# Kernel optimization log

Hardware: AMD Instinct MI355X
Metric: run time of the kernel (lower is better)

Reference implementation:

```python
import jax, jax.numpy as jnp
import numpy as np

NUM_NODES = 50000
FEAT_DIM = 64
HIDDEN = 128
OUT_DIM = 128
NUM_EDGES = 640000


def setup_inputs() -> dict:
    key = jax.random.key(0)
    ks = jax.random.split(key, 8)
    edge_index = jax.random.randint(ks[0], (2, NUM_EDGES), 0, NUM_NODES, dtype=jnp.int32)
    emb = jax.random.normal(ks[1], (NUM_NODES, FEAT_DIM), dtype=jnp.float32) * 0.1
    # SAGEConv: lin_l (aggregated neighbors, with bias) and lin_r (root, no bias)
    s1 = 1.0 / np.sqrt(FEAT_DIM)
    W1l = jax.random.uniform(ks[2], (HIDDEN, FEAT_DIM), jnp.float32, -s1, s1)
    b1l = jnp.zeros((HIDDEN,), jnp.float32)
    W1r = jax.random.uniform(ks[3], (HIDDEN, FEAT_DIM), jnp.float32, -s1, s1)
    s2 = 1.0 / np.sqrt(HIDDEN)
    W2l = jax.random.uniform(ks[4], (OUT_DIM, HIDDEN), jnp.float32, -s2, s2)
    b2l = jnp.zeros((OUT_DIM,), jnp.float32)
    W2r = jax.random.uniform(ks[5], (OUT_DIM, HIDDEN), jnp.float32, -s2, s2)
    return {"edge_index": edge_index, "emb": emb, "W1l": W1l, "b1l": b1l,
            "W1r": W1r, "W2l": W2l, "b2l": b2l, "W2r": W2r}


def _sage_conv(x, src, dst, Wl, bl, Wr):
    # mean-aggregate source features at target nodes, then two linear paths
    msg = x[src]                                   # [E, d]
    agg = jax.ops.segment_sum(msg, dst, num_segments=NUM_NODES)
    deg = jax.ops.segment_sum(jnp.ones((src.shape[0],), x.dtype), dst,
                              num_segments=NUM_NODES)
    mean = agg / jnp.maximum(deg, 1.0)[:, None]    # [N, d]
    return mean @ Wl.T + bl + x @ Wr.T             # [N, out]


def reference(edge_index, emb, W1l, b1l, W1r, W2l, b2l, W2r):
    src, dst = edge_index[0], edge_index[1]
    h = jax.nn.relu(_sage_conv(emb, src, dst, W1l, b1l, W1r))
    return _sage_conv(h, src, dst, W2l, b2l, W2r)
```

## Files before the change

### kernel.cpp

```cpp
#include <hip/hip_runtime.h>

#define N_NODES 50000
#define FEAT    64
#define HID     128
#define N_EDGES 640000
#define SBLK    196
#define CAP     80

typedef __attribute__((ext_vector_type(8))) short bf16x8;
typedef __attribute__((ext_vector_type(4))) float f32x4;

static __device__ __forceinline__ unsigned short f2bf(float f) {
    unsigned u = __float_as_uint(f);
    u = u + 0x7fffu + ((u >> 16) & 1u);
    return (unsigned short)(u >> 16);
}
static __device__ __forceinline__ float bflo(unsigned u) {
    return __uint_as_float(u << 16);
}
static __device__ __forceinline__ float bfhi(unsigned u) {
    return __uint_as_float(u & 0xffff0000u);
}

#define ACC8(A, v) { \
    A[0] += bflo((v).x); A[1] += bfhi((v).x); \
    A[2] += bflo((v).y); A[3] += bfhi((v).y); \
    A[4] += bflo((v).z); A[5] += bfhi((v).z); \
    A[6] += bflo((v).w); A[7] += bfhi((v).w); }

static __device__ __forceinline__ void gridbar(int* bar, int gen) {
    __syncthreads();
    if (threadIdx.x == 0) {
        __threadfence();
        int arrived = atomicAdd(&bar[0], 1);
        if (arrived == SBLK - 1) {
            atomicExch(&bar[0], 0);
            __threadfence();
            atomicExch(&bar[1], gen);
        } else {
            while (atomicAdd(&bar[1], 0) < gen) __builtin_amdgcn_s_sleep(2);
        }
        __threadfence();
    }
    __syncthreads();
}

__global__ __launch_bounds__(256) void histfill_kernel(
        const int* __restrict__ src, const int* __restrict__ dst,
        const float* __restrict__ emb,
        const float* __restrict__ W1l, const float* __restrict__ W1r,
        const float* __restrict__ W2l, const float* __restrict__ W2r,
        int* __restrict__ count, int* __restrict__ esrc,
        unsigned* __restrict__ emb_bf_u, unsigned* __restrict__ Wbf_u,
        unsigned* __restrict__ hbf_u) {
    int gtid = blockIdx.x * 256 + threadIdx.x;
    if (gtid < N_EDGES) {
        int d = dst[gtid];
        int slot = atomicAdd(&count[d], 1);
        if (slot < CAP) esrc[d * CAP + slot] = src[gtid];
    }
    for (int i = gtid; i < N_NODES * FEAT / 2; i += N_EDGES) {
        float2 v = ((const float2*)emb)[i];
        emb_bf_u[i] = ((unsigned)f2bf(v.y) << 16) | (unsigned)f2bf(v.x);
    }
    if (gtid < FEAT / 2) emb_bf_u[N_NODES * FEAT / 2 + gtid] = 0u;
    if (gtid < HID / 2)  hbf_u[N_NODES * HID / 2 + gtid]   = 0u;
    if (gtid < 24576) {
        int w = gtid * 2;
        float lo, hi;
        if (w < 8192)       { lo = W1l[w];         hi = W1l[w + 1]; }
        else if (w < 16384) { lo = W1r[w - 8192];  hi = W1r[w - 8191]; }
        else if (w < 32768) { lo = W2l[w - 16384]; hi = W2l[w - 16383]; }
        else                { lo = W2r[w - 32768]; hi = W2r[w - 32767]; }
        Wbf_u[gtid] = ((unsigned)f2bf(hi) << 16) | (unsigned)f2bf(lo);
    }
}

__global__ __launch_bounds__(256) void permk_kernel(
        const int* __restrict__ count, int* dhist, int* dcur, int* perm,
        int* bar) {
    __shared__ int lh[64];
    __shared__ int lb2[64];
    __shared__ int dstart_sh[64];
    __shared__ int scan_tmp[64];
    int t = threadIdx.x;
    int gtid = blockIdx.x * 256 + t;

    int v = (gtid < N_NODES) ? count[gtid] : 0;
    int d = v < 63 ? v : 63;
    if (t < 64) lh[t] = 0;
    __syncthreads();
    int slot = 0;
    if (gtid < N_NODES) slot = atomicAdd(&lh[d], 1);
    __syncthreads();
    if (t < 64 && lh[t] > 0) atomicAdd(&dhist[t], lh[t]);
    gridbar(bar, 1);

    int dv = (t < 64) ? dhist[t] : 0;
    if (t < 64) scan_tmp[t] = dv;
    __syncthreads();
    for (int off = 1; off < 64; off <<= 1) {
        int add = (t >= off && t < 64) ? scan_tmp[t - off] : 0;
        __syncthreads();
        if (t < 64) scan_tmp[t] += add;
        __syncthreads();
    }
    if (t < 64) dstart_sh[t] = scan_tmp[t] - dv;
    __syncthreads();
    if (t < 64 && lh[t] > 0) lb2[t] = atomicAdd(&dcur[t], lh[t]);
    __syncthreads();
    if (gtid < N_NODES)
        perm[(N_NODES - 1) - (dstart_sh[d] + lb2[d] + slot)] = gtid;
}

__global__ __launch_bounds__(256, 4) void fgemm1_kernel(
        const unsigned short* __restrict__ embb, const int* __restrict__ cnt,
        const int* __restrict__ esrc, const int* __restrict__ perm,
        const short* __restrict__ Wl, const short* __restrict__ Wr,
        const float* __restrict__ bias, unsigned short* __restrict__ hout) {
    __shared__ unsigned short smean[16][72];
    __shared__ int sidx[16][CAP];
    __shared__ int nid[16];
    int t = threadIdx.x;
    if (t < 16) nid[t] = perm[blockIdx.x * 16 + t];
    __syncthreads();

    int sub = t >> 4, fl = t & 15;
    int half = (t >> 3) & 1, fo = t & 7;
    int n = nid[sub];
    int deg = cnt[n];
    int degc = deg < CAP ? deg : CAP;
    int beg = n * CAP;
    int rr = (degc + 15) & ~15;
    for (int j = fl; j < rr; j += 16)
        sidx[sub][j] = (j < degc) ? esrc[beg + j] : N_NODES;
    float acc[8] = {0,0,0,0,0,0,0,0};
    const uint4* eb4 = (const uint4*)embb;
    for (int i = 0; i < rr; i += 16) {
        uint4 v0 = eb4[(size_t)sidx[sub][i +  0 + half] * 8 + fo];
        uint4 v1 = eb4[(size_t)sidx[sub][i +  2 + half] * 8 + fo];
        uint4 v2 = eb4[(size_t)sidx[sub][i +  4 + half] * 8 + fo];
        uint4 v3 = eb4[(size_t)sidx[sub][i +  6 + half] * 8 + fo];
        uint4 v4 = eb4[(size_t)sidx[sub][i +  8 + half] * 8 + fo];
        uint4 v5 = eb4[(size_t)sidx[sub][i + 10 + half] * 8 + fo];
        uint4 v6 = eb4[(size_t)sidx[sub][i + 12 + half] * 8 + fo];
        uint4 v7 = eb4[(size_t)sidx[sub][i + 14 + half] * 8 + fo];
        ACC8(acc, v0) ACC8(acc, v1) ACC8(acc, v2) ACC8(acc, v3)
        ACC8(acc, v4) ACC8(acc, v5) ACC8(acc, v6) ACC8(acc, v7)
    }
    float dinv = 1.0f / fmaxf((float)deg, 1.0f);
    unsigned ow[4];
    #pragma unroll
    for (int k = 0; k < 4; ++k) {
        float lo = acc[2 * k];     lo += __shfl_xor(lo, 8);
        float hi = acc[2 * k + 1]; hi += __shfl_xor(hi, 8);
        ow[k] = ((unsigned)f2bf(hi * dinv) << 16) | (unsigned)f2bf(lo * dinv);
    }
    if (half == 0) {
        uint4 o4 = {ow[0], ow[1], ow[2], ow[3]};
        *(uint4*)&smean[sub][fo * 8] = o4;
    }
    __syncthreads();

    int wave = t >> 6, lane = t & 63;
    int col = lane & 15, quad = lane >> 4;
    int ncol = nid[col];
    int nt0 = wave * 2, nt1 = nt0 + 1;
    f32x4 acc0 = (f32x4){0.f,0.f,0.f,0.f}, acc1 = (f32x4){0.f,0.f,0.f,0.f};
    #pragma unroll
    for (int kb = 0; kb < FEAT; kb += 32) {
        bf16x8 am = *(const bf16x8*)&smean[col][kb + quad * 8];
        bf16x8 ax = *(const bf16x8*)(embb + (size_t)ncol * FEAT + kb + quad * 8);
        bf16x8 bl0 = *(const bf16x8*)(Wl + (nt0 * 16 + col) * FEAT + kb + quad * 8);
        bf16x8 br0 = *(const bf16x8*)(Wr + (nt0 * 16 + col) * FEAT + kb + quad * 8);
        bf16x8 bl1 = *(const bf16x8*)(Wl + (nt1 * 16 + col) * FEAT + kb + quad * 8);
        bf16x8 br1 = *(const bf16x8*)(Wr + (nt1 * 16 + col) * FEAT + kb + quad * 8);
        acc0 = __builtin_amdgcn_mfma_f32_16x16x32_bf16(am, bl0, acc0, 0, 0, 0);
        acc0 = __builtin_amdgcn_mfma_f32_16x16x32_bf16(ax, br0, acc0, 0, 0, 0);
        acc1 = __builtin_amdgcn_mfma_f32_16x16x32_bf16(am, bl1, acc1, 0, 0, 0);
        acc1 = __builtin_amdgcn_mfma_f32_16x16x32_bf16(ax, br1, acc1, 0, 0, 0);
    }
    float bv0 = bias[nt0 * 16 + col];
    float bv1 = bias[nt1 * 16 + col];
    #pragma unroll
    for (int r = 0; r < 4; ++r) {
        int node = nid[quad * 4 + r];
        hout[(size_t)node * HID + nt0 * 16 + col] = f2bf(fmaxf(acc0[r] + bv0, 0.f));
        hout[(size_t)node * HID + nt1 * 16 + col] = f2bf(fmaxf(acc1[r] + bv1, 0.f));
    }
}

__global__ __launch_bounds__(256, 4) void fgemm2_kernel(
        const unsigned short* __restrict__ hbf, const int* __restrict__ cnt,
        const int* __restrict__ esrc, const int* __restrict__ perm,
        const short* __restrict__ Wl, const short* __restrict__ Wr,
        const float* __restrict__ bias, float* __restrict__ out) {
    __shared__ unsigned short smean[16][136];
    __shared__ int sidx[16][CAP];
    __shared__ int nid[16];
    int t = threadIdx.x;
    if (t < 16) nid[t] = perm[blockIdx.x * 16 + t];
    __syncthreads();

    int sub = t >> 4, fl = t & 15;
    int n = nid[sub];
    int deg = cnt[n];
    int degc = deg < CAP ? deg : CAP;
    int beg = n * CAP;
    int rr = (degc + 7) & ~7;
    for (int j = fl; j < rr; j += 16)
        sidx[sub][j] = (j < degc) ? esrc[beg + j] : N_NODES;
    float acc[8] = {0,0,0,0,0,0,0,0};
    const uint4* hb4 = (const uint4*)hbf;
    for (int i = 0; i < rr; i += 8) {
        uint4 v0 = hb4[(size_t)sidx[sub][i + 0] * 16 + fl];
        uint4 v1 = hb4[(size_t)sidx[sub][i + 1] * 16 + fl];
        uint4 v2 = hb4[(size_t)sidx[sub][i + 2] * 16 + fl];
        uint4 v3 = hb4[(size_t)sidx[sub][i + 3] * 16 + fl];
        uint4 v4 = hb4[(size_t)sidx[sub][i + 4] * 16 + fl];
        uint4 v5 = hb4[(size_t)sidx[sub][i + 5] * 16 + fl];
        uint4 v6 = hb4[(size_t)sidx[sub][i + 6] * 16 + fl];
        uint4 v7 = hb4[(size_t)sidx[sub][i + 7] * 16 + fl];
        ACC8(acc, v0) ACC8(acc, v1) ACC8(acc, v2) ACC8(acc, v3)
        ACC8(acc, v4) ACC8(acc, v5) ACC8(acc, v6) ACC8(acc, v7)
    }
    float dinv = 1.0f / fmaxf((float)deg, 1.0f);
    unsigned ow[4];
    #pragma unroll
    for (int k = 0; k < 4; ++k) {
        float lo = acc[2 * k] * dinv;
        float hi = acc[2 * k + 1] * dinv;
        ow[k] = ((unsigned)f2bf(hi) << 16) | (unsigned)f2bf(lo);
    }
    uint4 o4 = {ow[0], ow[1], ow[2], ow[3]};
    *(uint4*)&smean[sub][fl * 8] = o4;
    __syncthreads();

    int wave = t >> 6, lane = t & 63;
    int col = lane & 15, quad = lane >> 4;
    int ncol = nid[col];
    int nt0 = wave * 2, nt1 = nt0 + 1;
    f32x4 acc0 = (f32x4){0.f,0.f,0.f,0.f}, acc1 = (f32x4){0.f,0.f,0.f,0.f};
    #pragma unroll
    for (int kb = 0; kb < HID; kb += 32) {
        bf16x8 am = *(const bf16x8*)&smean[col][kb + quad * 8];
        bf16x8 ax = *(const bf16x8*)(hbf + (size_t)ncol * HID + kb + quad * 8);
        bf16x8 bl0 = *(const bf16x8*)(Wl + (nt0 * 16 + col) * HID + kb + quad * 8);
        bf16x8 br0 = *(const bf16x8*)(Wr + (nt0 * 16 + col) * HID + kb + quad * 8);
        bf16x8 bl1 = *(const bf16x8*)(Wl + (nt1 * 16 + col) * HID + kb + quad * 8);
        bf16x8 br1 = *(const bf16x8*)(Wr + (nt1 * 16 + col) * HID + kb + quad * 8);
        acc0 = __builtin_amdgcn_mfma_f32_16x16x32_bf16(am, bl0, acc0, 0, 0, 0);
        acc0 = __builtin_amdgcn_mfma_f32_16x16x32_bf16(ax, br0, acc0, 0, 0, 0);
        acc1 = __builtin_amdgcn_mfma_f32_16x16x32_bf16(am, bl1, acc1, 0, 0, 0);
        acc1 = __builtin_amdgcn_mfma_f32_16x16x32_bf16(ax, br1, acc1, 0, 0, 0);
    }
    float bv0 = bias[nt0 * 16 + col];
    float bv1 = bias[nt1 * 16 + col];
    #pragma unroll
    for (int r = 0; r < 4; ++r) {
        int node = nid[quad * 4 + r];
        out[(size_t)node * HID + nt0 * 16 + col] = acc0[r] + bv0;
        out[(size_t)node * HID + nt1 * 16 + col] = acc1[r] + bv1;
    }
}

extern "C" void kernel_launch(void* const* d_in, const int* in_sizes, int n_in,
                              void* d_out, int out_size, void* d_ws, size_t ws_size,
                              hipStream_t stream) {
    const int*   edge_index = (const int*)d_in[0];
    const float* emb        = (const float*)d_in[1];
    const float* W1l        = (const float*)d_in[2];
    const float* b1l        = (const float*)d_in[3];
    const float* W1r        = (const float*)d_in[4];
    const float* W2l        = (const float*)d_in[5];
    const float* b2l        = (const float*)d_in[6];
    const float* W2r        = (const float*)d_in[7];
    float* out = (float*)d_out;

    const int* src = edge_index;
    const int* dst = edge_index + N_EDGES;

    int* iws    = (int*)d_ws;
    int* count  = iws;
    int* dhist  = iws + 50000;
    int* dcur   = iws + 50064;
    int* bar    = iws + 50128;
    int* perm   = iws + 50132;
    int* esrc   = iws + 100132;
    unsigned short* W1l_bf = (unsigned short*)(iws + 4100132);
    unsigned short* W1r_bf = (unsigned short*)(iws + 4104228);
    unsigned short* W2l_bf = (unsigned short*)(iws + 4108324);
    unsigned short* W2r_bf = (unsigned short*)(iws + 4116516);
    unsigned short* Wbf    = W1l_bf;
    unsigned short* emb_bf = (unsigned short*)(iws + 4124708);
    unsigned short* hbf    = (unsigned short*)(iws + 5724740);

    (void)hipMemsetAsync(count, 0, (size_t)50132 * sizeof(int), stream);

    histfill_kernel<<<(N_EDGES + 255) / 256, 256, 0, stream>>>(
        src, dst, emb, W1l, W1r, W2l, W2r, count, esrc,
        (unsigned*)emb_bf, (unsigned*)Wbf, (unsigned*)hbf);
    permk_kernel<<<SBLK, 256, 0, stream>>>(
        count, dhist, dcur, perm, bar);

    fgemm1_kernel<<<N_NODES / 16, 256, 0, stream>>>(
        emb_bf, count, esrc, perm,
        (const short*)W1l_bf, (const short*)W1r_bf, b1l, hbf);
    fgemm2_kernel<<<N_NODES / 16, 256, 0, stream>>>(
        hbf, count, esrc, perm,
        (const short*)W2l_bf, (const short*)W2r_bf, b2l, out);
}
```

Before: 219.1 us.

## Fuse all stages into one persistent kernel with grid barriers

Replaces the histogram/fill, permutation, and two gather+GEMM kernels with a single persistent kernel of 256 blocks of 1024 threads, separated by software grid barriers. Each block processes four 16-node tiles at once over several rounds. This removes kernel launch gaps and inter-kernel drain, but adds barrier latency and reduces the number of resident waves available to hide gather latency.

```diff
diff --git a/kernel.cpp b/kernel.cpp
--- a/kernel.cpp
+++ b/kernel.cpp
@@ -4,7 +4,10 @@
 #define FEAT    64
 #define HID     128
 #define N_EDGES 640000
-#define SBLK    196
+#define MBLK    256
+#define MTHR    1024
+#define NT      3125
+#define NROUND  4
 #define CAP     80
 
 typedef __attribute__((ext_vector_type(8))) short bf16x8;
@@ -33,7 +36,7 @@
     if (threadIdx.x == 0) {
         __threadfence();
         int arrived = atomicAdd(&bar[0], 1);
-        if (arrived == SBLK - 1) {
+        if (arrived == MBLK - 1) {
             atomicExch(&bar[0], 0);
             __threadfence();
             atomicExch(&bar[1], gen);
@@ -45,21 +48,33 @@
     __syncthreads();
 }
 
-__global__ __launch_bounds__(256) void histfill_kernel(
+__global__ __launch_bounds__(MTHR, 4) void mega_kernel(
         const int* __restrict__ src, const int* __restrict__ dst,
         const float* __restrict__ emb,
         const float* __restrict__ W1l, const float* __restrict__ W1r,
         const float* __restrict__ W2l, const float* __restrict__ W2r,
-        int* __restrict__ count, int* __restrict__ esrc,
+        const float* __restrict__ b1l, const float* __restrict__ b2l,
+        int* __restrict__ count, int* dhist, int* dcur, int* perm,
+        int* __restrict__ esrc, int* bar,
         unsigned* __restrict__ emb_bf_u, unsigned* __restrict__ Wbf_u,
-        unsigned* __restrict__ hbf_u) {
-    int gtid = blockIdx.x * 256 + threadIdx.x;
-    if (gtid < N_EDGES) {
-        int d = dst[gtid];
+        unsigned* __restrict__ hbf_u,
+        const short* __restrict__ W1l_bf, const short* __restrict__ W1r_bf,
+        const short* __restrict__ W2l_bf, const short* __restrict__ W2r_bf,
+        float* __restrict__ out) {
+    __shared__ unsigned short smean[4][16][136];
+    __shared__ int sidx[4][16][CAP];
+    __shared__ int nid[4][16];
+    __shared__ int lh[64], lb2[64], dstart_sh[64], scan_tmp[64];
+    int t = threadIdx.x;
+    int gtid = blockIdx.x * MTHR + t;
+    const int GRID = MBLK * MTHR;
+
+    for (int e = gtid; e < N_EDGES; e += GRID) {
+        int d = dst[e];
         int slot = atomicAdd(&count[d], 1);
-        if (slot < CAP) esrc[d * CAP + slot] = src[gtid];
-    }
-    for (int i = gtid; i < N_NODES * FEAT / 2; i += N_EDGES) {
+        if (slot < CAP) esrc[d * CAP + slot] = src[e];
+    }
+    for (int i = gtid; i < N_NODES * FEAT / 2; i += GRID) {
         float2 v = ((const float2*)emb)[i];
         emb_bf_u[i] = ((unsigned)f2bf(v.y) << 16) | (unsigned)f2bf(v.x);
     }
@@ -74,193 +89,185 @@
         else                { lo = W2r[w - 32768]; hi = W2r[w - 32767]; }
         Wbf_u[gtid] = ((unsigned)f2bf(hi) << 16) | (unsigned)f2bf(lo);
     }
-}
-
-__global__ __launch_bounds__(256) void permk_kernel(
-        const int* __restrict__ count, int* dhist, int* dcur, int* perm,
-        int* bar) {
-    __shared__ int lh[64];
-    __shared__ int lb2[64];
-    __shared__ int dstart_sh[64];
-    __shared__ int scan_tmp[64];
-    int t = threadIdx.x;
-    int gtid = blockIdx.x * 256 + t;
-
-    int v = (gtid < N_NODES) ? count[gtid] : 0;
-    int d = v < 63 ? v : 63;
-    if (t < 64) lh[t] = 0;
-    __syncthreads();
-    int slot = 0;
-    if (gtid < N_NODES) slot = atomicAdd(&lh[d], 1);
-    __syncthreads();
-    if (t < 64 && lh[t] > 0) atomicAdd(&dhist[t], lh[t]);
     gridbar(bar, 1);
 
-    int dv = (t < 64) ? dhist[t] : 0;
-    if (t < 64) scan_tmp[t] = dv;
-    __syncthreads();
-    for (int off = 1; off < 64; off <<= 1) {
-        int add = (t >= off && t < 64) ? scan_tmp[t - off] : 0;
-        __syncthreads();
-        if (t < 64) scan_tmp[t] += add;
-        __syncthreads();
-    }
-    if (t < 64) dstart_sh[t] = scan_tmp[t] - dv;
-    __syncthreads();
-    if (t < 64 && lh[t] > 0) lb2[t] = atomicAdd(&dcur[t], lh[t]);
-    __syncthreads();
-    if (gtid < N_NODES)
-        perm[(N_NODES - 1) - (dstart_sh[d] + lb2[d] + slot)] = gtid;
-}
-
-__global__ __launch_bounds__(256, 4) void fgemm1_kernel(
-        const unsigned short* __restrict__ embb, const int* __restrict__ cnt,
-        const int* __restrict__ esrc, const int* __restrict__ perm,
-        const short* __restrict__ Wl, const short* __restrict__ Wr,
-        const float* __restrict__ bias, unsigned short* __restrict__ hout) {
-    __shared__ unsigned short smean[16][72];
-    __shared__ int sidx[16][CAP];
-    __shared__ int nid[16];
-    int t = threadIdx.x;
-    if (t < 16) nid[t] = perm[blockIdx.x * 16 + t];
-    __syncthreads();
-
-    int sub = t >> 4, fl = t & 15;
-    int half = (t >> 3) & 1, fo = t & 7;
-    int n = nid[sub];
-    int deg = cnt[n];
-    int degc = deg < CAP ? deg : CAP;
-    int beg = n * CAP;
-    int rr = (degc + 15) & ~15;
-    for (int j = fl; j < rr; j += 16)
-        sidx[sub][j] = (j < degc) ? esrc[beg + j] : N_NODES;
-    float acc[8] = {0,0,0,0,0,0,0,0};
-    const uint4* eb4 = (const uint4*)embb;
-    for (int i = 0; i < rr; i += 16) {
-        uint4 v0 = eb4[(size_t)sidx[sub][i +  0 + half] * 8 + fo];
-        uint4 v1 = eb4[(size_t)sidx[sub][i +  2 + half] * 8 + fo];
-        uint4 v2 = eb4[(size_t)sidx[sub][i +  4 + half] * 8 + fo];
-        uint4 v3 = eb4[(size_t)sidx[sub][i +  6 + half] * 8 + fo];
-        uint4 v4 = eb4[(size_t)sidx[sub][i +  8 + half] * 8 + fo];
-        uint4 v5 = eb4[(size_t)sidx[sub][i + 10 + half] * 8 + fo];
-        uint4 v6 = eb4[(size_t)sidx[sub][i + 12 + half] * 8 + fo];
-        uint4 v7 = eb4[(size_t)sidx[sub][i + 14 + half] * 8 + fo];
-        ACC8(acc, v0) ACC8(acc, v1) ACC8(acc, v2) ACC8(acc, v3)
-        ACC8(acc, v4) ACC8(acc, v5) ACC8(acc, v6) ACC8(acc, v7)
-    }
-    float dinv = 1.0f / fmaxf((float)deg, 1.0f);
-    unsigned ow[4];
-    #pragma unroll
-    for (int k = 0; k < 4; ++k) {
-        float lo = acc[2 * k];     lo += __shfl_xor(lo, 8);
-        float hi = acc[2 * k + 1]; hi += __shfl_xor(hi, 8);
-        ow[k] = ((unsigned)f2bf(hi * dinv) << 16) | (unsigned)f2bf(lo * dinv);
-    }
-    if (half == 0) {
-        uint4 o4 = {ow[0], ow[1], ow[2], ow[3]};
-        *(uint4*)&smean[sub][fo * 8] = o4;
-    }
-    __syncthreads();
-
-    int wave = t >> 6, lane = t & 63;
-    int col = lane & 15, quad = lane >> 4;
-    int ncol = nid[col];
-    int nt0 = wave * 2, nt1 = nt0 + 1;
-    f32x4 acc0 = (f32x4){0.f,0.f,0.f,0.f}, acc1 = (f32x4){0.f,0.f,0.f,0.f};
-    #pragma unroll
-    for (int kb = 0; kb < FEAT; kb += 32) {
-        bf16x8 am = *(const bf16x8*)&smean[col][kb + quad * 8];
-        bf16x8 ax = *(const bf16x8*)(embb + (size_t)ncol * FEAT + kb + quad * 8);
-        bf16x8 bl0 = *(const bf16x8*)(Wl + (nt0 * 16 + col) * FEAT + kb + quad * 8);
-        bf16x8 br0 = *(const bf16x8*)(Wr + (nt0 * 16 + col) * FEAT + kb + quad * 8);
-        bf16x8 bl1 = *(const bf16x8*)(Wl + (nt1 * 16 + col) * FEAT + kb + quad * 8);
-        bf16x8 br1 = *(const bf16x8*)(Wr + (nt1 * 16 + col) * FEAT + kb + quad * 8);
-        acc0 = __builtin_amdgcn_mfma_f32_16x16x32_bf16(am, bl0, acc0, 0, 0, 0);
-        acc0 = __builtin_amdgcn_mfma_f32_16x16x32_bf16(ax, br0, acc0, 0, 0, 0);
-        acc1 = __builtin_amdgcn_mfma_f32_16x16x32_bf16(am, bl1, acc1, 0, 0, 0);
-        acc1 = __builtin_amdgcn_mfma_f32_16x16x32_bf16(ax, br1, acc1, 0, 0, 0);
-    }
-    float bv0 = bias[nt0 * 16 + col];
-    float bv1 = bias[nt1 * 16 + col];
-    #pragma unroll
-    for (int r = 0; r < 4; ++r) {
-        int node = nid[quad * 4 + r];
-        hout[(size_t)node * HID + nt0 * 16 + col] = f2bf(fmaxf(acc0[r] + bv0, 0.f));
-        hout[(size_t)node * HID + nt1 * 16 + col] = f2bf(fmaxf(acc1[r] + bv1, 0.f));
-    }
-}
-
-__global__ __launch_bounds__(256, 4) void fgemm2_kernel(
-        const unsigned short* __restrict__ hbf, const int* __restrict__ cnt,
-        const int* __restrict__ esrc, const int* __restrict__ perm,
-        const short* __restrict__ Wl, const short* __restrict__ Wr,
-        const float* __restrict__ bias, float* __restrict__ out) {
-    __shared__ unsigned short smean[16][136];
-    __shared__ int sidx[16][CAP];
-    __shared__ int nid[16];
-    int t = threadIdx.x;
-    if (t < 16) nid[t] = perm[blockIdx.x * 16 + t];
-    __syncthreads();
-
-    int sub = t >> 4, fl = t & 15;
-    int n = nid[sub];
-    int deg = cnt[n];
-    int degc = deg < CAP ? deg : CAP;
-    int beg = n * CAP;
-    int rr = (degc + 7) & ~7;
-    for (int j = fl; j < rr; j += 16)
-        sidx[sub][j] = (j < degc) ? esrc[beg + j] : N_NODES;
-    float acc[8] = {0,0,0,0,0,0,0,0};
-    const uint4* hb4 = (const uint4*)hbf;
-    for (int i = 0; i < rr; i += 8) {
-        uint4 v0 = hb4[(size_t)sidx[sub][i + 0] * 16 + fl];
-        uint4 v1 = hb4[(size_t)sidx[sub][i + 1] * 16 + fl];
-        uint4 v2 = hb4[(size_t)sidx[sub][i + 2] * 16 + fl];
-        uint4 v3 = hb4[(size_t)sidx[sub][i + 3] * 16 + fl];
-        uint4 v4 = hb4[(size_t)sidx[sub][i + 4] * 16 + fl];
-        uint4 v5 = hb4[(size_t)sidx[sub][i + 5] * 16 + fl];
-        uint4 v6 = hb4[(size_t)sidx[sub][i + 6] * 16 + fl];
-        uint4 v7 = hb4[(size_t)sidx[sub][i + 7] * 16 + fl];
-        ACC8(acc, v0) ACC8(acc, v1) ACC8(acc, v2) ACC8(acc, v3)
-        ACC8(acc, v4) ACC8(acc, v5) ACC8(acc, v6) ACC8(acc, v7)
-    }
-    float dinv = 1.0f / fmaxf((float)deg, 1.0f);
-    unsigned ow[4];
-    #pragma unroll
-    for (int k = 0; k < 4; ++k) {
-        float lo = acc[2 * k] * dinv;
-        float hi = acc[2 * k + 1] * dinv;
-        ow[k] = ((unsigned)f2bf(hi) << 16) | (unsigned)f2bf(lo);
-    }
-    uint4 o4 = {ow[0], ow[1], ow[2], ow[3]};
-    *(uint4*)&smean[sub][fl * 8] = o4;
-    __syncthreads();
-
-    int wave = t >> 6, lane = t & 63;
-    int col = lane & 15, quad = lane >> 4;
-    int ncol = nid[col];
-    int nt0 = wave * 2, nt1 = nt0 + 1;
-    f32x4 acc0 = (f32x4){0.f,0.f,0.f,0.f}, acc1 = (f32x4){0.f,0.f,0.f,0.f};
-    #pragma unroll
-    for (int kb = 0; kb < HID; kb += 32) {
-        bf16x8 am = *(const bf16x8*)&smean[col][kb + quad * 8];
-        bf16x8 ax = *(const bf16x8*)(hbf + (size_t)ncol * HID + kb + quad * 8);
-        bf16x8 bl0 = *(const bf16x8*)(Wl + (nt0 * 16 + col) * HID + kb + quad * 8);
-        bf16x8 br0 = *(const bf16x8*)(Wr + (nt0 * 16 + col) * HID + kb + quad * 8);
-        bf16x8 bl1 = *(const bf16x8*)(Wl + (nt1 * 16 + col) * HID + kb + quad * 8);
-        bf16x8 br1 = *(const bf16x8*)(Wr + (nt1 * 16 + col) * HID + kb + quad * 8);
-        acc0 = __builtin_amdgcn_mfma_f32_16x16x32_bf16(am, bl0, acc0, 0, 0, 0);
-        acc0 = __builtin_amdgcn_mfma_f32_16x16x32_bf16(ax, br0, acc0, 0, 0, 0);
-        acc1 = __builtin_amdgcn_mfma_f32_16x16x32_bf16(am, bl1, acc1, 0, 0, 0);
-        acc1 = __builtin_amdgcn_mfma_f32_16x16x32_bf16(ax, br1, acc1, 0, 0, 0);
-    }
-    float bv0 = bias[nt0 * 16 + col];
-    float bv1 = bias[nt1 * 16 + col];
-    #pragma unroll
-    for (int r = 0; r < 4; ++r) {
-        int node = nid[quad * 4 + r];
-        out[(size_t)node * HID + nt0 * 16 + col] = acc0[r] + bv0;
-        out[(size_t)node * HID + nt1 * 16 + col] = acc1[r] + bv1;
+    {
+        int v = (gtid < N_NODES) ? count[gtid] : 0;
+        int d = v < 63 ? v : 63;
+        if (t < 64) lh[t] = 0;
+        __syncthreads();
+        int slot = 0;
+        if (gtid < N_NODES) slot = atomicAdd(&lh[d], 1);
+        __syncthreads();
+        if (t < 64 && lh[t] > 0) atomicAdd(&dhist[t], lh[t]);
+        gridbar(bar, 2);
+        int dv = (t < 64) ? dhist[t] : 0;
+        if (t < 64) scan_tmp[t] = dv;
+        __syncthreads();
+        for (int off = 1; off < 64; off <<= 1) {
+            int add = (t >= off && t < 64) ? scan_tmp[t - off] : 0;
+            __syncthreads();
+            if (t < 64) scan_tmp[t] += add;
+            __syncthreads();
+        }
+        if (t < 64) dstart_sh[t] = scan_tmp[t] - dv;
+        __syncthreads();
+        if (t < 64 && lh[t] > 0) lb2[t] = atomicAdd(&dcur[t], lh[t]);
+        __syncthreads();
+        if (gtid < N_NODES)
+            perm[(N_NODES - 1) - (dstart_sh[d] + lb2[d] + slot)] = gtid;
+    }
+    gridbar(bar, 3);
+
+    int q = t >> 8, tq = t & 255;
+
+    {
+        int sub = tq >> 4, fl = tq & 15;
+        int half = (tq >> 3) & 1, fo = tq & 7;
+        const unsigned short* embb = (const unsigned short*)emb_bf_u;
+        const uint4* eb4 = (const uint4*)embb;
+        for (int r = 0; r < NROUND; ++r) {
+            int tile = r * (MBLK * 4) + blockIdx.x * 4 + q;
+            bool active = tile < NT;
+            if (active && tq < 16) nid[q][tq] = perm[tile * 16 + tq];
+            __syncthreads();
+            int n = N_NODES, deg = 0;
+            if (active) { n = nid[q][sub]; deg = count[n]; }
+            int degc = deg < CAP ? deg : CAP;
+            int beg = n * CAP;
+            int rr = (degc + 15) & ~15;
+            for (int j = fl; j < rr; j += 16)
+                sidx[q][sub][j] = (j < degc) ? esrc[beg + j] : N_NODES;
+            float acc[8] = {0,0,0,0,0,0,0,0};
+            for (int i = 0; i < rr; i += 16) {
+                uint4 v0 = eb4[(size_t)sidx[q][sub][i +  0 + half] * 8 + fo];
+                uint4 v1 = eb4[(size_t)sidx[q][sub][i +  2 + half] * 8 + fo];
+                uint4 v2 = eb4[(size_t)sidx[q][sub][i +  4 + half] * 8 + fo];
+                uint4 v3 = eb4[(size_t)sidx[q][sub][i +  6 + half] * 8 + fo];
+                uint4 v4 = eb4[(size_t)sidx[q][sub][i +  8 + half] * 8 + fo];
+                uint4 v5 = eb4[(size_t)sidx[q][sub][i + 10 + half] * 8 + fo];
+                uint4 v6 = eb4[(size_t)sidx[q][sub][i + 12 + half] * 8 + fo];
+                uint4 v7 = eb4[(size_t)sidx[q][sub][i + 14 + half] * 8 + fo];
+                ACC8(acc, v0) ACC8(acc, v1) ACC8(acc, v2) ACC8(acc, v3)
+                ACC8(acc, v4) ACC8(acc, v5) ACC8(acc, v6) ACC8(acc, v7)
+            }
+            float dinv = 1.0f / fmaxf((float)deg, 1.0f);
+            unsigned ow[4];
+            #pragma unroll
+            for (int k = 0; k < 4; ++k) {
+                float lo = acc[2 * k];     lo += __shfl_xor(lo, 8);
+                float hi = acc[2 * k + 1]; hi += __shfl_xor(hi, 8);
+                ow[k] = ((unsigned)f2bf(hi * dinv) << 16) | (unsigned)f2bf(lo * dinv);
+            }
+            if (half == 0) {
+                uint4 o4 = {ow[0], ow[1], ow[2], ow[3]};
+                *(uint4*)&smean[q][sub][fo * 8] = o4;
+            }
+            __syncthreads();
+            if (active) {
+                int wave = tq >> 6, lane = tq & 63;
+                int col = lane & 15, quad = lane >> 4;
+                int ncol = nid[q][col];
+                int nt0 = wave * 2, nt1 = nt0 + 1;
+                f32x4 a0 = (f32x4){0.f,0.f,0.f,0.f}, a1 = (f32x4){0.f,0.f,0.f,0.f};
+                #pragma unroll
+                for (int kb = 0; kb < FEAT; kb += 32) {
+                    bf16x8 am = *(const bf16x8*)&smean[q][col][kb + quad * 8];
+                    bf16x8 ax = *(const bf16x8*)(embb + (size_t)ncol * FEAT + kb + quad * 8);
+                    bf16x8 bl0 = *(const bf16x8*)(W1l_bf + (nt0 * 16 + col) * FEAT + kb + quad * 8);
+                    bf16x8 br0 = *(const bf16x8*)(W1r_bf + (nt0 * 16 + col) * FEAT + kb + quad * 8);
+                    bf16x8 bl1 = *(const bf16x8*)(W1l_bf + (nt1 * 16 + col) * FEAT + kb + quad * 8);
+                    bf16x8 br1 = *(const bf16x8*)(W1r_bf + (nt1 * 16 + col) * FEAT + kb + quad * 8);
+                    a0 = __builtin_amdgcn_mfma_f32_16x16x32_bf16(am, bl0, a0, 0, 0, 0);
+                    a0 = __builtin_amdgcn_mfma_f32_16x16x32_bf16(ax, br0, a0, 0, 0, 0);
+                    a1 = __builtin_amdgcn_mfma_f32_16x16x32_bf16(am, bl1, a1, 0, 0, 0);
+                    a1 = __builtin_amdgcn_mfma_f32_16x16x32_bf16(ax, br1, a1, 0, 0, 0);
+                }
+                unsigned short* hout = (unsigned short*)hbf_u;
+                float bv0 = b1l[nt0 * 16 + col];
+                float bv1 = b1l[nt1 * 16 + col];
+                #pragma unroll
+                for (int k = 0; k < 4; ++k) {
+                    int node = nid[q][quad * 4 + k];
+                    hout[(size_t)node * HID + nt0 * 16 + col] = f2bf(fmaxf(a0[k] + bv0, 0.f));
+                    hout[(size_t)node * HID + nt1 * 16 + col] = f2bf(fmaxf(a1[k] + bv1, 0.f));
+                }
+            }
+            __syncthreads();
+        }
+    }
+    gridbar(bar, 4);
+
+    {
+        int sub = tq >> 4, fl = tq & 15;
+        const unsigned short* hbf = (const unsigned short*)hbf_u;
+        const uint4* hb4 = (const uint4*)hbf;
+        for (int r = 0; r < NROUND; ++r) {
+            int tile = r * (MBLK * 4) + blockIdx.x * 4 + q;
+            bool active = tile < NT;
+            if (active && tq < 16) nid[q][tq] = perm[tile * 16 + tq];
+            __syncthreads();
+            int n = N_NODES, deg = 0;
+            if (active) { n = nid[q][sub]; deg = count[n]; }
+            int degc = deg < CAP ? deg : CAP;
+            int beg = n * CAP;
+            int rr = (degc + 7) & ~7;
+            for (int j = fl; j < rr; j += 16)
+                sidx[q][sub][j] = (j < degc) ? esrc[beg + j] : N_NODES;
+            float acc[8] = {0,0,0,0,0,0,0,0};
+            for (int i = 0; i < rr; i += 8) {
+                uint4 v0 = hb4[(size_t)sidx[q][sub][i + 0] * 16 + fl];
+                uint4 v1 = hb4[(size_t)sidx[q][sub][i + 1] * 16 + fl];
+                uint4 v2 = hb4[(size_t)sidx[q][sub][i + 2] * 16 + fl];
+                uint4 v3 = hb4[(size_t)sidx[q][sub][i + 3] * 16 + fl];
+                uint4 v4 = hb4[(size_t)sidx[q][sub][i + 4] * 16 + fl];
+                uint4 v5 = hb4[(size_t)sidx[q][sub][i + 5] * 16 + fl];
+                uint4 v6 = hb4[(size_t)sidx[q][sub][i + 6] * 16 + fl];
+                uint4 v7 = hb4[(size_t)sidx[q][sub][i + 7] * 16 + fl];
+                ACC8(acc, v0) ACC8(acc, v1) ACC8(acc, v2) ACC8(acc, v3)
+                ACC8(acc, v4) ACC8(acc, v5) ACC8(acc, v6) ACC8(acc, v7)
+            }
+            float dinv = 1.0f / fmaxf((float)deg, 1.0f);
+            unsigned ow[4];
+            #pragma unroll
+            for (int k = 0; k < 4; ++k) {
+                float lo = acc[2 * k] * dinv;
+                float hi = acc[2 * k + 1] * dinv;
+                ow[k] = ((unsigned)f2bf(hi) << 16) | (unsigned)f2bf(lo);
+            }
+            uint4 o4 = {ow[0], ow[1], ow[2], ow[3]};
+            *(uint4*)&smean[q][sub][fl * 8] = o4;
+            __syncthreads();
+            if (active) {
+                int wave = tq >> 6, lane = tq & 63;
+                int col = lane & 15, quad = lane >> 4;
+                int ncol = nid[q][col];
+                int nt0 = wave * 2, nt1 = nt0 + 1;
+                f32x4 a0 = (f32x4){0.f,0.f,0.f,0.f}, a1 = (f32x4){0.f,0.f,0.f,0.f};
+                #pragma unroll
+                for (int kb = 0; kb < HID; kb += 32) {
+                    bf16x8 am = *(const bf16x8*)&smean[q][col][kb + quad * 8];
+                    bf16x8 ax = *(const bf16x8*)(hbf + (size_t)ncol * HID + kb + quad * 8);
+                    bf16x8 bl0 = *(const bf16x8*)(W2l_bf + (nt0 * 16 + col) * HID + kb + quad * 8);
+                    bf16x8 br0 = *(const bf16x8*)(W2r_bf + (nt0 * 16 + col) * HID + kb + quad * 8);
+                    bf16x8 bl1 = *(const bf16x8*)(W2l_bf + (nt1 * 16 + col) * HID + kb + quad * 8);
+                    bf16x8 br1 = *(const bf16x8*)(W2r_bf + (nt1 * 16 + col) * HID + kb + quad * 8);
+                    a0 = __builtin_amdgcn_mfma_f32_16x16x32_bf16(am, bl0, a0, 0, 0, 0);
+                    a0 = __builtin_amdgcn_mfma_f32_16x16x32_bf16(ax, br0, a0, 0, 0, 0);
+                    a1 = __builtin_amdgcn_mfma_f32_16x16x32_bf16(am, bl1, a1, 0, 0, 0);
+                    a1 = __builtin_amdgcn_mfma_f32_16x16x32_bf16(ax, br1, a1, 0, 0, 0);
+                }
+                float bv0 = b2l[nt0 * 16 + col];
+                float bv1 = b2l[nt1 * 16 + col];
+                #pragma unroll
+                for (int k = 0; k < 4; ++k) {
+                    int node = nid[q][quad * 4 + k];
+                    out[(size_t)node * HID + nt0 * 16 + col] = a0[k] + bv0;
+                    out[(size_t)node * HID + nt1 * 16 + col] = a1[k] + bv1;
+                }
+            }
+            __syncthreads();
+        }
     }
 }
 
@@ -297,16 +304,10 @@
 
     (void)hipMemsetAsync(count, 0, (size_t)50132 * sizeof(int), stream);
 
-    histfill_kernel<<<(N_EDGES + 255) / 256, 256, 0, stream>>>(
-        src, dst, emb, W1l, W1r, W2l, W2r, count, esrc,
-        (unsigned*)emb_bf, (unsigned*)Wbf, (unsigned*)hbf);
-    permk_kernel<<<SBLK, 256, 0, stream>>>(
-        count, dhist, dcur, perm, bar);
-
-    fgemm1_kernel<<<N_NODES / 16, 256, 0, stream>>>(
-        emb_bf, count, esrc, perm,
-        (const short*)W1l_bf, (const short*)W1r_bf, b1l, hbf);
-    fgemm2_kernel<<<N_NODES / 16, 256, 0, stream>>>(
-        hbf, count, esrc, perm,
-        (const short*)W2l_bf, (const short*)W2r_bf, b2l, out);
-}
+    mega_kernel<<<MBLK, MTHR, 0, stream>>>(
+        src, dst, emb, W1l, W1r, W2l, W2r, b1l, b2l,
+        count, dhist, dcur, perm, esrc, bar,
+        (unsigned*)emb_bf, (unsigned*)Wbf, (unsigned*)hbf,
+        (const short*)W1l_bf, (const short*)W1r_bf,
+        (const short*)W2l_bf, (const short*)W2r_bf, out);
+}
```

Result: slower. 323.6 us (+47.7%).

## Fuse histogram fill and degree-sort permutation into one persistent kernel

Applied to the files above, without the earlier changes.

Merges the edge-bucketing/bf16 conversion kernel and the degree-bucket permutation kernel into a single persistent kernel of 256 blocks of 1024 threads, with grid-stride loops and an extra software grid barrier between phases. This removes one kernel launch and its inter-kernel gap. The cost is an additional spin-wait grid barrier, and correctness depends on all 256 large blocks being co-resident.

```diff
diff --git a/kernel.cpp b/kernel.cpp
--- a/kernel.cpp
+++ b/kernel.cpp
@@ -4,7 +4,8 @@
 #define FEAT    64
 #define HID     128
 #define N_EDGES 640000
-#define SBLK    196
+#define PBLK    256
+#define PTHR    1024
 #define CAP     80
 
 typedef __attribute__((ext_vector_type(8))) short bf16x8;
@@ -33,7 +34,7 @@
     if (threadIdx.x == 0) {
         __threadfence();
         int arrived = atomicAdd(&bar[0], 1);
-        if (arrived == SBLK - 1) {
+        if (arrived == PBLK - 1) {
             atomicExch(&bar[0], 0);
             __threadfence();
             atomicExch(&bar[1], gen);
@@ -45,21 +46,26 @@
     __syncthreads();
 }
 
-__global__ __launch_bounds__(256) void histfill_kernel(
+__global__ __launch_bounds__(PTHR, 4) void prep_kernel(
         const int* __restrict__ src, const int* __restrict__ dst,
         const float* __restrict__ emb,
         const float* __restrict__ W1l, const float* __restrict__ W1r,
         const float* __restrict__ W2l, const float* __restrict__ W2r,
-        int* __restrict__ count, int* __restrict__ esrc,
+        int* __restrict__ count, int* dhist, int* dcur, int* perm,
+        int* __restrict__ esrc, int* bar,
         unsigned* __restrict__ emb_bf_u, unsigned* __restrict__ Wbf_u,
         unsigned* __restrict__ hbf_u) {
-    int gtid = blockIdx.x * 256 + threadIdx.x;
-    if (gtid < N_EDGES) {
-        int d = dst[gtid];
+    __shared__ int lh[64], lb2[64], dstart_sh[64], scan_tmp[64];
+    int t = threadIdx.x;
+    int gtid = blockIdx.x * PTHR + t;
+    const int GRID = PBLK * PTHR;
+
+    for (int e = gtid; e < N_EDGES; e += GRID) {
+        int d = dst[e];
         int slot = atomicAdd(&count[d], 1);
-        if (slot < CAP) esrc[d * CAP + slot] = src[gtid];
-    }
-    for (int i = gtid; i < N_NODES * FEAT / 2; i += N_EDGES) {
+        if (slot < CAP) esrc[d * CAP + slot] = src[e];
+    }
+    for (int i = gtid; i < N_NODES * FEAT / 2; i += GRID) {
         float2 v = ((const float2*)emb)[i];
         emb_bf_u[i] = ((unsigned)f2bf(v.y) << 16) | (unsigned)f2bf(v.x);
     }
@@ -74,17 +80,7 @@
         else                { lo = W2r[w - 32768]; hi = W2r[w - 32767]; }
         Wbf_u[gtid] = ((unsigned)f2bf(hi) << 16) | (unsigned)f2bf(lo);
     }
-}
-
-__global__ __launch_bounds__(256) void permk_kernel(
-        const int* __restrict__ count, int* dhist, int* dcur, int* perm,
-        int* bar) {
-    __shared__ int lh[64];
-    __shared__ int lb2[64];
-    __shared__ int dstart_sh[64];
-    __shared__ int scan_tmp[64];
-    int t = threadIdx.x;
-    int gtid = blockIdx.x * 256 + t;
+    gridbar(bar, 1);
 
     int v = (gtid < N_NODES) ? count[gtid] : 0;
     int d = v < 63 ? v : 63;
@@ -94,7 +90,7 @@
     if (gtid < N_NODES) slot = atomicAdd(&lh[d], 1);
     __syncthreads();
     if (t < 64 && lh[t] > 0) atomicAdd(&dhist[t], lh[t]);
-    gridbar(bar, 1);
+    gridbar(bar, 2);
 
     int dv = (t < 64) ? dhist[t] : 0;
     if (t < 64) scan_tmp[t] = dv;
@@ -297,11 +293,10 @@
 
     (void)hipMemsetAsync(count, 0, (size_t)50132 * sizeof(int), stream);
 
-    histfill_kernel<<<(N_EDGES + 255) / 256, 256, 0, stream>>>(
-        src, dst, emb, W1l, W1r, W2l, W2r, count, esrc,
+    prep_kernel<<<PBLK, PTHR, 0, stream>>>(
+        src, dst, emb, W1l, W1r, W2l, W2r,
+        count, dhist, dcur, perm, esrc, bar,
         (unsigned*)emb_bf, (unsigned*)Wbf, (unsigned*)hbf);
-    permk_kernel<<<SBLK, 256, 0, stream>>>(
-        count, dhist, dcur, perm, bar);
 
     fgemm1_kernel<<<N_NODES / 16, 256, 0, stream>>>(
         emb_bf, count, esrc, perm,
```

Result: slower. 254.8 us (+16.3%).
